# Kernel optimization log

Measured on AMD Instinct MI355X. Metric: run time of the kernel, lower is better.

## Reference

```python
import jax, jax.numpy as jnp
import numpy as np

N, E, D_IN, D, H, L, D_EMB, T = 4096, 131072, 72, 256, 8, 2, 128, 5
HD = D // H
LN_EPS = 1e-5


def _linear(x, w, b):
    # torch Linear: w is [out, in]
    return x @ w.T + b


def _layernorm(x, g, b):
    mu = jnp.mean(x, axis=-1, keepdims=True)
    var = jnp.var(x, axis=-1, keepdims=True)
    return (x - mu) * jax.lax.rsqrt(var + LN_EPS) * g + b


def _gps_layer(x, edge_index, p):
    src, dst = edge_index[0], edge_index[1]
    # GINConv: sum-aggregate neighbor messages, then MLP((1+eps)*x + agg)
    agg = jax.ops.segment_sum(x[src], dst, num_segments=N)
    h = (1.0 + p['gin_eps']) * x + agg
    h = _linear(jax.nn.elu(_linear(h, p['mlp_w1'], p['mlp_b1'])), p['mlp_w2'], p['mlp_b2'])
    h = jax.nn.elu(_layernorm(h, p['ln1_g'], p['ln1_b']))
    x = x + h

    # global multi-head self-attention over all N nodes (seq len = N)
    qkv = x @ p['attn_in_w'].T + p['attn_in_b']  # [N, 3D]
    q, k, v = jnp.split(qkv, 3, axis=-1)
    q = q.reshape(N, H, HD)
    k = k.reshape(N, H, HD)
    v = v.reshape(N, H, HD)
    scores = jnp.einsum('nhd,mhd->hnm', q, k) / np.sqrt(HD).astype(np.float32)
    attn = jax.nn.softmax(scores, axis=-1)
    o = jnp.einsum('hnm,mhd->nhd', attn, v).reshape(N, D)
    o = _linear(o, p['attn_out_w'], p['attn_out_b'])
    o = _layernorm(o, p['ln2_g'], p['ln2_b'])
    x = x + o

    # FFN (dim -> 2*dim -> dim, GELU)
    f = _linear(jax.nn.gelu(_linear(x, p['ffn_w1'], p['ffn_b1'])), p['ffn_w2'], p['ffn_b2'])
    f = _layernorm(f, p['ln3_g'], p['ln3_b'])
    return x + f


def setup_inputs() -> dict:
    key = jax.random.key(0)
    ks = iter(jax.random.split(key, 64))

    def w(shape, fan_in):
        return jax.random.normal(next(ks), shape, jnp.float32) * (1.0 / np.sqrt(fan_in))

    inp = {
        'x': jax.random.normal(next(ks), (N, D_IN), jnp.float32),
        'edge_index': jax.random.randint(next(ks), (2, E), 0, N, jnp.int64),
        'in_w': w((D, D_IN), D_IN), 'in_b': jnp.zeros((D,), jnp.float32),
        'head_w1': w((D_EMB, D), D), 'head_b1': jnp.zeros((D_EMB,), jnp.float32),
        'head_w2': w((T, D_EMB), D_EMB), 'head_b2': jnp.zeros((T,), jnp.float32),
    }
    # stacked per-layer params, leading axis L
    inp['mlp_w1'] = w((L, D, D), D); inp['mlp_b1'] = jnp.zeros((L, D), jnp.float32)
    inp['mlp_w2'] = w((L, D, D), D); inp['mlp_b2'] = jnp.zeros((L, D), jnp.float32)
    inp['gin_eps'] = jnp.zeros((L,), jnp.float32)
    inp['ln1_g'] = jnp.ones((L, D), jnp.float32); inp['ln1_b'] = jnp.zeros((L, D), jnp.float32)
    inp['attn_in_w'] = w((L, 3 * D, D), D); inp['attn_in_b'] = jnp.zeros((L, 3 * D), jnp.float32)
    inp['attn_out_w'] = w((L, D, D), D); inp['attn_out_b'] = jnp.zeros((L, D), jnp.float32)
    inp['ln2_g'] = jnp.ones((L, D), jnp.float32); inp['ln2_b'] = jnp.zeros((L, D), jnp.float32)
    inp['ffn_w1'] = w((L, 2 * D, D), D); inp['ffn_b1'] = jnp.zeros((L, 2 * D), jnp.float32)
    inp['ffn_w2'] = w((L, D, 2 * D), 2 * D); inp['ffn_b2'] = jnp.zeros((L, D), jnp.float32)
    inp['ln3_g'] = jnp.ones((L, D), jnp.float32); inp['ln3_b'] = jnp.zeros((L, D), jnp.float32)
    return inp


PER_LAYER = ['mlp_w1', 'mlp_b1', 'mlp_w2', 'mlp_b2', 'gin_eps', 'ln1_g', 'ln1_b',
             'attn_in_w', 'attn_in_b', 'attn_out_w', 'attn_out_b', 'ln2_g', 'ln2_b',
             'ffn_w1', 'ffn_b1', 'ffn_w2', 'ffn_b2', 'ln3_g', 'ln3_b']


def reference(x, edge_index, in_w, in_b, head_w1, head_b1, head_w2, head_b2,
              mlp_w1, mlp_b1, mlp_w2, mlp_b2, gin_eps, ln1_g, ln1_b,
              attn_in_w, attn_in_b, attn_out_w, attn_out_b, ln2_g, ln2_b,
              ffn_w1, ffn_b1, ffn_w2, ffn_b2, ln3_g, ln3_b):
    stacked = dict(mlp_w1=mlp_w1, mlp_b1=mlp_b1, mlp_w2=mlp_w2, mlp_b2=mlp_b2,
                   gin_eps=gin_eps, ln1_g=ln1_g, ln1_b=ln1_b,
                   attn_in_w=attn_in_w, attn_in_b=attn_in_b,
                   attn_out_w=attn_out_w, attn_out_b=attn_out_b,
                   ln2_g=ln2_g, ln2_b=ln2_b, ffn_w1=ffn_w1, ffn_b1=ffn_b1,
                   ffn_w2=ffn_w2, ffn_b2=ffn_b2, ln3_g=ln3_g, ln3_b=ln3_b)
    h = jax.nn.elu(_linear(x, in_w, in_b))  # input_proj (dropout/noise off in eval)
    for l in range(L):
        p = {k: v[l] for k, v in stacked.items()}
        h = _gps_layer(h, edge_index, p)
    out = _linear(jax.nn.elu(_linear(h, head_w1, head_b1)), head_w2, head_b2)
    return out
```

## Files before the change

kernel.cpp:

```cpp
#include <hip/hip_runtime.h>
#include <hip/hip_bf16.h>
#include <math.h>

#define NN 4096
#define NE 131072
#define DIM 256
#define NHEAD 8
#define HD 32

typedef __attribute__((ext_vector_type(8))) short short8v;
typedef __attribute__((ext_vector_type(4))) float f32x4;
#define MFMA16(a, b, c) __builtin_amdgcn_mfma_f32_16x16x32_bf16(a, b, c, 0, 0, 0)

__device__ __forceinline__ float elu_f(float v){ return v > 0.f ? v : expm1f(v); }
__device__ __forceinline__ float gelu_f(float v){
  const float c = 0.7978845608028654f;
  float t = tanhf(c * (v + 0.044715f * v * v * v));
  return 0.5f * v * (1.f + t);
}
__device__ __forceinline__ unsigned short f2bf(float f) {
  unsigned int u = __builtin_bit_cast(unsigned int, f);
  u += 0x7FFFu + ((u >> 16) & 1u);
  return (unsigned short)(u >> 16);
}
__device__ __forceinline__ float bf2f(unsigned short u) {
  return __builtin_bit_cast(float, (unsigned int)u << 16);
}
__device__ __forceinline__ unsigned int pk2c(float a, float b) {
  __hip_bfloat162 h = __float22bfloat162_rn(float2{a, b});
  unsigned int r;
  __builtin_memcpy(&r, &h, 4);
  return r;
}

__global__ void zero_counts(int* __restrict__ counts) {
  int i = blockIdx.x * 256 + threadIdx.x;
  if (i < NN) counts[i] = 0;
}

__global__ void count_edges(const int* __restrict__ ei, int* __restrict__ counts) {
  int e = blockIdx.x * 256 + threadIdx.x;
  if (e < NE) atomicAdd(&counts[ei[NE + e]], 1);
}

__global__ __launch_bounds__(1024) void scan_offsets(const int* __restrict__ counts,
                                                     int* __restrict__ offs,
                                                     int* __restrict__ cursor) {
  __shared__ int tmp[1024];
  int t = threadIdx.x;
  int base = t * 4;
  int c0 = counts[base], c1 = counts[base+1], c2 = counts[base+2], c3 = counts[base+3];
  int tsum = c0 + c1 + c2 + c3;
  tmp[t] = tsum;
  __syncthreads();
  for (int d = 1; d < 1024; d <<= 1) {
    int v = (t >= d) ? tmp[t - d] : 0;
    __syncthreads();
    tmp[t] += v;
    __syncthreads();
  }
  int excl = tmp[t] - tsum;
  offs[base]   = excl;           cursor[base]   = excl;
  offs[base+1] = excl + c0;      cursor[base+1] = excl + c0;
  offs[base+2] = excl + c0 + c1; cursor[base+2] = excl + c0 + c1;
  offs[base+3] = excl + c0 + c1 + c2; cursor[base+3] = excl + c0 + c1 + c2;
  if (t == 1023) offs[NN] = tmp[1023];
}

__global__ void scatter_edges(const int* __restrict__ ei, int* __restrict__ cursor,
                              int* __restrict__ esrc) {
  int e = blockIdx.x * 256 + threadIdx.x;
  if (e < NE) {
    int d = ei[NE + e];
    int pos = atomicAdd(&cursor[d], 1);
    esrc[pos] = ei[e];
  }
}

__global__ __launch_bounds__(256) void gin_agg(const int* __restrict__ offs,
                                               const int* __restrict__ esrc,
                                               const unsigned short* __restrict__ xb,
                                               const float* __restrict__ eps_p, int l,
                                               unsigned short* __restrict__ aggb) {
  int n = blockIdx.x, c = threadIdx.x;
  int e0 = offs[n], e1 = offs[n + 1];
  float acc = 0.f;
  for (int e = e0; e < e1; e++) acc += bf2f(xb[(size_t)esrc[e] * DIM + c]);
  float eps = eps_p[l];
  aggb[(size_t)n * DIM + c] = f2bf((1.f + eps) * bf2f(xb[(size_t)n * DIM + c]) + acc);
}

template<int ACT, int WF32, int WBF16, int QSCALE, int BK>
__global__ __launch_bounds__(256) void gemm_mfma(
    const unsigned short* __restrict__ A, const unsigned short* __restrict__ W,
    const float* __restrict__ bias, float* __restrict__ Cf,
    unsigned short* __restrict__ Cb, int M, int N, int K)
{
  __shared__ __align__(16) unsigned short As[2][64][BK + 8];
  __shared__ __align__(16) unsigned short Ws[2][32][BK + 8];
  constexpr int CPR = BK / 8;
  constexpr int ACH = 64 * CPR;
  constexpr int WCH = 32 * CPR;
  constexpr int NA = (ACH + 255) / 256;
  constexpr int NW = (WCH + 255) / 256;
  int t = threadIdx.x;
  int w = t >> 6, lane = t & 63, lo = lane & 15, g = lane >> 4;
  int wm = w & 1, wn = w >> 1;
  int bn = blockIdx.x * 32, bm = blockIdx.y * 64;

  f32x4 acc0 = {0.f, 0.f, 0.f, 0.f};
  f32x4 acc1 = {0.f, 0.f, 0.f, 0.f};
  short8v pa[NA], pw[NW];

  auto LOADG = [&](int k0) {
    #pragma unroll
    for (int i = 0; i < NA; i++) {
      int cc = i * 256 + t;
      int row = cc / CPR, off = (cc % CPR) * 8;
      pa[i] = *(const short8v*)(A + (size_t)(bm + row) * K + k0 + off);
    }
    #pragma unroll
    for (int i = 0; i < NW; i++) {
      int cc = i * 256 + t;
      if (cc < WCH) {
        int row = cc / CPR, off = (cc % CPR) * 8;
        pw[i] = *(const short8v*)(W + (size_t)(bn + row) * K + k0 + off);
      }
    }
  };
  auto STORE = [&](int b) {
    #pragma unroll
    for (int i = 0; i < NA; i++) {
      int cc = i * 256 + t;
      int row = cc / CPR, off = (cc % CPR) * 8;
      *(short8v*)&As[b][row][off] = pa[i];
    }
    #pragma unroll
    for (int i = 0; i < NW; i++) {
      int cc = i * 256 + t;
      if (cc < WCH) {
        int row = cc / CPR, off = (cc % CPR) * 8;
        *(short8v*)&Ws[b][row][off] = pw[i];
      }
    }
  };

  LOADG(0);
  STORE(0);
  __syncthreads();

  int buf = 0;
  for (int k0 = 0; k0 < K; k0 += BK) {
    bool more = (k0 + BK < K);
    if (more) LOADG(k0 + BK);
    #pragma unroll
    for (int ks = 0; ks < BK; ks += 32) {
      short8v a0 = *(const short8v*)&As[buf][wm * 32 + lo][ks + 8 * g];
      short8v a1 = *(const short8v*)&As[buf][wm * 32 + 16 + lo][ks + 8 * g];
      short8v b0 = *(const short8v*)&Ws[buf][wn * 16 + lo][ks + 8 * g];
      acc0 = MFMA16(a0, b0, acc0);
      acc1 = MFMA16(a1, b0, acc1);
    }
    if (more) STORE(buf ^ 1);
    __syncthreads();
    buf ^= 1;
  }

  #pragma unroll
  for (int mi = 0; mi < 2; mi++) {
    f32x4 av = (mi == 0) ? acc0 : acc1;
    #pragma unroll
    for (int r = 0; r < 4; r++) {
      int row = bm + wm * 32 + mi * 16 + 4 * g + r;
      int col = bn + wn * 16 + lo;
      float v = av[r] + bias[col];
      if (ACT == 1) v = elu_f(v);
      if (ACT == 2) v = gelu_f(v);
      if (QSCALE) { if (col < 256) v *= 0.17677669529663687f; }
      if (WF32) Cf[(size_t)row * N + col] = v;
      if (WBF16) Cb[(size_t)row * N + col] = f2bf(v);
    }
  }
}

template<int ACT>
__global__ __launch_bounds__(256) void ln_act_add(const float* __restrict__ in,
                                                  const float* __restrict__ g,
                                                  const float* __restrict__ b,
                                                  float* __restrict__ x,
                                                  unsigned short* __restrict__ xb) {
  int rowb = blockIdx.x;
  int c = threadIdx.x;
  float v = in[(size_t)rowb * DIM + c];
  float s = v, s2 = v * v;
  #pragma unroll
  for (int off = 32; off >= 1; off >>= 1) {
    s  += __shfl_xor(s,  off, 64);
    s2 += __shfl_xor(s2, off, 64);
  }
  __shared__ float ws1[4], ws2[4];
  int w = threadIdx.x >> 6, lane = threadIdx.x & 63;
  if (lane == 0) { ws1[w] = s; ws2[w] = s2; }
  __syncthreads();
  s  = ws1[0] + ws1[1] + ws1[2] + ws1[3];
  s2 = ws2[0] + ws2[1] + ws2[2] + ws2[3];
  float mean = s * (1.f / DIM);
  float var = s2 * (1.f / DIM) - mean * mean;
  float r = rsqrtf(var + 1e-5f);
  float o = (v - mean) * r * g[c] + b[c];
  if (ACT == 1) o = elu_f(o);
  float nx = x[(size_t)rowb * DIM + c] + o;
  x[(size_t)rowb * DIM + c] = nx;
  xb[(size_t)rowb * DIM + c] = f2bf(nx);
}

__global__ __launch_bounds__(256) void vt_transpose(const unsigned short* __restrict__ tbb,
                                                    unsigned short* __restrict__ VT) {
  __shared__ unsigned short lds[128][33];
  int h = blockIdx.y;
  int nb = blockIdx.x * 128;
  int tid = threadIdx.x;
  int r8 = tid >> 5, d = tid & 31;
  #pragma unroll
  for (int i = 0; i < 16; i++) {
    int n = i * 8 + r8;
    lds[n][d] = tbb[(size_t)(nb + n) * 768 + 512 + h * 32 + d];
  }
  __syncthreads();
  int dd = tid >> 7, j = tid & 127;
  #pragma unroll
  for (int i = 0; i < 16; i++) {
    int d2 = i * 2 + dd;
    VT[((size_t)h * 32 + d2) * 4096 + nb + j] = lds[j][d2];
  }
}

__global__ __launch_bounds__(256) void attn_mfma_split(
    const unsigned short* __restrict__ qkvb, const unsigned short* __restrict__ VT,
    float* __restrict__ po, float* __restrict__ ml, int kspan) {
  __shared__ __align__(16) unsigned short Ks[2][64][40];
  __shared__ __align__(16) unsigned short Vs[2][32][72];
  int tid = threadIdx.x;
  int w = tid >> 6, lane = tid & 63;
  int lo = lane & 15, g = lane >> 4;
  int h = blockIdx.y;
  int s = blockIdx.z;
  int qb = blockIdx.x * 64 + w * 16;
  int k_lo = s * kspan, k_hi = k_lo + kspan;

  int krow = tid >> 2, kq = (tid & 3) * 8;
  int vrow = tid >> 3, vo = (tid & 7) * 8;
  const unsigned short* Kg = qkvb + 256 + h * 32;
  const unsigned short* Vg = VT + ((size_t)(h * 32 + vrow)) * 4096;

  short8v qf = *(const short8v*)(qkvb + (size_t)(qb + lo) * 768 + h * 32 + 8 * g);

  f32x4 acc0 = {0.f, 0.f, 0.f, 0.f};
  f32x4 acc1 = {0.f, 0.f, 0.f, 0.f};
  float m = -1e30f, l = 0.f;
  const f32x4 zf = {0.f, 0.f, 0.f, 0.f};

  {
    short8v rk0 = *(const short8v*)(Kg + (size_t)(k_lo + krow) * 768 + kq);
    short8v rv0 = *(const short8v*)(Vg + k_lo + vo);
    *(short8v*)&Ks[0][krow][kq] = rk0;
    *(short8v*)&Vs[0][vrow][vo] = rv0;
  }
  __syncthreads();

  int buf = 0;
  for (int kb = k_lo; kb < k_hi; kb += 64) {
    short8v rk, rv;
    bool more = (kb + 64 < k_hi);
    if (more) {
      rk = *(const short8v*)(Kg + (size_t)(kb + 64 + krow) * 768 + kq);
      rv = *(const short8v*)(Vg + kb + 64 + vo);
    }

    short8v kA0 = *(const short8v*)&Ks[buf][lo][8 * g];
    short8v kA1 = *(const short8v*)&Ks[buf][16 + lo][8 * g];
    short8v kA2 = *(const short8v*)&Ks[buf][32 + lo][8 * g];
    short8v kA3 = *(const short8v*)&Ks[buf][48 + lo][8 * g];
    f32x4 s0_ = MFMA16(kA0, qf, zf);
    f32x4 s1_ = MFMA16(kA1, qf, zf);
    f32x4 s2_ = MFMA16(kA2, qf, zf);
    f32x4 s3_ = MFMA16(kA3, qf, zf);

    float ta_ = fmaxf(fmaxf(fmaxf(s0_[0],s0_[1]), fmaxf(s0_[2],s0_[3])),
                      fmaxf(fmaxf(s1_[0],s1_[1]), fmaxf(s1_[2],s1_[3])));
    float tb_ = fmaxf(fmaxf(fmaxf(s2_[0],s2_[1]), fmaxf(s2_[2],s2_[3])),
                      fmaxf(fmaxf(s3_[0],s3_[1]), fmaxf(s3_[2],s3_[3])));
    float t_ = fmaxf(ta_, tb_);
    t_ = fmaxf(t_, __shfl_xor(t_, 16, 64));
    t_ = fmaxf(t_, __shfl_xor(t_, 32, 64));
    if (!__all(t_ <= m)) {
      float nm_ = fmaxf(m, t_);
      float f_ = __expf(m - nm_);
      m = nm_; l *= f_;
      acc0[0]*=f_; acc0[1]*=f_; acc0[2]*=f_; acc0[3]*=f_;
      acc1[0]*=f_; acc1[1]*=f_; acc1[2]*=f_; acc1[3]*=f_;
    }
    float p0_=__expf(s0_[0]-m), p1_=__expf(s0_[1]-m), p2_=__expf(s0_[2]-m), p3_=__expf(s0_[3]-m);
    float p4_=__expf(s1_[0]-m), p5_=__expf(s1_[1]-m), p6_=__expf(s1_[2]-m), p7_=__expf(s1_[3]-m);
    float p8_=__expf(s2_[0]-m), p9_=__expf(s2_[1]-m), pA_=__expf(s2_[2]-m), pB_=__expf(s2_[3]-m);
    float pC_=__expf(s3_[0]-m), pD_=__expf(s3_[1]-m), pE_=__expf(s3_[2]-m), pF_=__expf(s3_[3]-m);
    l += ((((p0_+p1_)+(p2_+p3_)) + ((p4_+p5_)+(p6_+p7_))) +
          (((p8_+p9_)+(pA_+pB_)) + ((pC_+pD_)+(pE_+pF_))));

    uint4 uA_ = { pk2c(p0_,p1_), pk2c(p2_,p3_), pk2c(p4_,p5_), pk2c(p6_,p7_) };
    uint4 uB_ = { pk2c(p8_,p9_), pk2c(pA_,pB_), pk2c(pC_,pD_), pk2c(pE_,pF_) };
    short8v pbA_ = __builtin_bit_cast(short8v, uA_);
    short8v pbB_ = __builtin_bit_cast(short8v, uB_);

    short4 Wa0 = *(const short4*)&Vs[buf][lo][4 * g];
    short4 Wa1 = *(const short4*)&Vs[buf][lo][16 + 4 * g];
    short4 Wa2 = *(const short4*)&Vs[buf][lo][32 + 4 * g];
    short4 Wa3 = *(const short4*)&Vs[buf][lo][48 + 4 * g];
    short4 Xa0 = *(const short4*)&Vs[buf][16 + lo][4 * g];
    short4 Xa1 = *(const short4*)&Vs[buf][16 + lo][16 + 4 * g];
    short4 Xa2 = *(const short4*)&Vs[buf][16 + lo][32 + 4 * g];
    short4 Xa3 = *(const short4*)&Vs[buf][16 + lo][48 + 4 * g];
    short8v va0_ = {Wa0.x,Wa0.y,Wa0.z,Wa0.w, Wa1.x,Wa1.y,Wa1.z,Wa1.w};
    short8v va1_ = {Wa2.x,Wa2.y,Wa2.z,Wa2.w, Wa3.x,Wa3.y,Wa3.z,Wa3.w};
    short8v vb0_ = {Xa0.x,Xa0.y,Xa0.z,Xa0.w, Xa1.x,Xa1.y,Xa1.z,Xa1.w};
    short8v vb1_ = {Xa2.x,Xa2.y,Xa2.z,Xa2.w, Xa3.x,Xa3.y,Xa3.z,Xa3.w};
    acc0 = MFMA16(va0_, pbA_, acc0);
    acc0 = MFMA16(va1_, pbB_, acc0);
    acc1 = MFMA16(vb0_, pbA_, acc1);
    acc1 = MFMA16(vb1_, pbB_, acc1);

    if (more) {
      *(short8v*)&Ks[buf ^ 1][krow][kq] = rk;
      *(short8v*)&Vs[buf ^ 1][vrow][vo] = rv;
    }
    __syncthreads();
    buf ^= 1;
  }

  l += __shfl_xor(l, 16, 64);
  l += __shfl_xor(l, 32, 64);

  int q = qb + lo;
  float* pr = po + ((size_t)s * NN + q) * DIM + h * 32 + 4 * g;
  *(f32x4*)pr = acc0;
  *(f32x4*)(pr + 16) = acc1;
  if (g == 0) {
    float2* mlp = (float2*)(ml + (((size_t)s * NN + q) * NHEAD + h) * 2);
    *mlp = float2{m, l};
  }
}

__global__ __launch_bounds__(256) void attn_merge(const float* __restrict__ po,
                                                  const float* __restrict__ ml,
                                                  unsigned short* __restrict__ attb, int S) {
  int q = blockIdx.x;
  int c = threadIdx.x;
  int h = c >> 5;
  float M = -1e30f;
  for (int s = 0; s < S; s++)
    M = fmaxf(M, ml[(((size_t)s * NN + q) * NHEAD + h) * 2]);
  float L = 0.f, O = 0.f;
  for (int s = 0; s < S; s++) {
    const float* mlp = ml + (((size_t)s * NN + q) * NHEAD + h) * 2;
    float e = __expf(mlp[0] - M);
    L += e * mlp[1];
    O += e * po[((size_t)s * NN + q) * DIM + c];
  }
  attb[(size_t)q * DIM + c] = f2bf(O / L);
}

#define WO0 0
#define WO1 131072
#define WO2 262144
#define WO3 655360
#define WO4 786432
#define WO5 1048576
#define WO6 1310720
#define WTOT 1343488
#define WBLK 1312
#define XPBLK 1536
#define WPBLK 96
__global__ __launch_bounds__(256) void prep_convert(
    const float* __restrict__ s0, const float* __restrict__ s1,
    const float* __restrict__ s2, const float* __restrict__ s3,
    const float* __restrict__ s4, const float* __restrict__ s5,
    const float* __restrict__ s6, unsigned short* __restrict__ dst,
    const float* __restrict__ x_in, unsigned short* __restrict__ xinb,
    const float* __restrict__ in_w, unsigned short* __restrict__ inwb) {
  int bid = blockIdx.x;
  if (bid < WBLK) {
    int i4 = (bid * 256 + threadIdx.x) * 4;
    if (i4 >= WTOT) return;
    const float* src; int loc;
    if      (i4 < WO1) { src = s0; loc = i4 - WO0; }
    else if (i4 < WO2) { src = s1; loc = i4 - WO1; }
    else if (i4 < WO3) { src = s2; loc = i4 - WO2; }
    else if (i4 < WO4) { src = s3; loc = i4 - WO3; }
    else if (i4 < WO5) { src = s4; loc = i4 - WO4; }
    else if (i4 < WO6) { src = s5; loc = i4 - WO5; }
    else               { src = s6; loc = i4 - WO6; }
    float4 v = *(const float4*)(src + loc);
    ushort4 o;
    o.x = f2bf(v.x); o.y = f2bf(v.y); o.z = f2bf(v.z); o.w = f2bf(v.w);
    *(ushort4*)(dst + i4) = o;
  } else if (bid < WBLK + XPBLK) {
    int idx = (bid - WBLK) * 256 + threadIdx.x;
    int row = idx / 96, col = idx - row * 96;
    xinb[idx] = (col < 72) ? f2bf(x_in[row * 72 + col]) : (unsigned short)0;
  } else {
    int idx = (bid - WBLK - XPBLK) * 256 + threadIdx.x;
    int row = idx / 96, col = idx - row * 96;
    inwb[idx] = (col < 72) ? f2bf(in_w[row * 72 + col]) : (unsigned short)0;
  }
}

__global__ void head2_kernel(const float* __restrict__ e, const float* __restrict__ w,
                             const float* __restrict__ b, float* __restrict__ out) {
  int idx = blockIdx.x * 256 + threadIdx.x;
  if (idx >= NN * 5) return;
  int rowi = idx / 5, col = idx % 5;
  float s = b[col];
  const float* ep = e + (size_t)rowi * 128;
  const float* wp = w + (size_t)col * 128;
  #pragma unroll 16
  for (int k = 0; k < 128; k++) s += ep[k] * wp[k];
  out[idx] = s;
}

extern "C" void kernel_launch(void* const* d_in, const int* in_sizes, int n_in,
                              void* d_out, int out_size, void* d_ws, size_t ws_size,
                              hipStream_t stream) {
  const float* x_in   = (const float*)d_in[0];
  const int*   ei     = (const int*)  d_in[1];
  const float* in_w   = (const float*)d_in[2];
  const float* in_b   = (const float*)d_in[3];
  const float* head_w1= (const float*)d_in[4];
  const float* head_b1= (const float*)d_in[5];
  const float* head_w2= (const float*)d_in[6];
  const float* head_b2= (const float*)d_in[7];
  const float* mlp_w1 = (const float*)d_in[8];
  const float* mlp_b1 = (const float*)d_in[9];
  const float* mlp_w2 = (const float*)d_in[10];
  const float* mlp_b2 = (const float*)d_in[11];
  const float* gin_eps= (const float*)d_in[12];
  const float* ln1_g  = (const float*)d_in[13];
  const float* ln1_b  = (const float*)d_in[14];
  const float* attn_in_w = (const float*)d_in[15];
  const float* attn_in_b = (const float*)d_in[16];
  const float* attn_out_w= (const float*)d_in[17];
  const float* attn_out_b= (const float*)d_in[18];
  const float* ln2_g  = (const float*)d_in[19];
  const float* ln2_b  = (const float*)d_in[20];
  const float* ffn_w1 = (const float*)d_in[21];
  const float* ffn_b1 = (const float*)d_in[22];
  const float* ffn_w2 = (const float*)d_in[23];
  const float* ffn_b2 = (const float*)d_in[24];
  const float* ln3_g  = (const float*)d_in[25];
  const float* ln3_b  = (const float*)d_in[26];

  float* ws = (float*)d_ws;
  float* x    = ws;
  float* t2   = x  + (size_t)NN * DIM;
  float* he   = t2 + (size_t)NN * DIM;
  unsigned short* xb   = (unsigned short*)(he + (size_t)NN * 128);
  unsigned short* tbb  = xb   + (size_t)NN * DIM;
  unsigned short* aggb = tbb  + (size_t)NN * 768;
  unsigned short* attb = aggb + (size_t)NN * DIM;
  unsigned short* VT   = attb + (size_t)NN * DIM;
  unsigned short* xinb = VT   + (size_t)NN * DIM;
  unsigned short* inwb = xinb + (size_t)NN * 96;
  unsigned short* warena = inwb + 256 * 96;
  int* counts = (int*)(warena + WTOT);
  int* offs   = counts + NN;
  int* cursor = offs + NN + 1;
  int* esrc   = cursor + NN;
  float* po   = (float*)(esrc + NE);
  size_t used_f = (size_t)(po - ws);
  int S = 1;
  for (int cand = 8; cand >= 2; cand >>= 1) {
    size_t need = (used_f + (size_t)cand * NN * DIM + (size_t)cand * NN * NHEAD * 2) * 4;
    if (ws_size >= need) { S = cand; break; }
  }
  float* ml = po + (size_t)S * NN * DIM;
  int kspan = NN / S;

  const unsigned short* w_mlp1 = warena + WO0;
  const unsigned short* w_mlp2 = warena + WO1;
  const unsigned short* w_qkv  = warena + WO2;
  const unsigned short* w_aout = warena + WO3;
  const unsigned short* w_ffn1 = warena + WO4;
  const unsigned short* w_ffn2 = warena + WO5;
  const unsigned short* w_h1   = warena + WO6;

  zero_counts<<<16, 256, 0, stream>>>(counts);
  count_edges<<<NE / 256, 256, 0, stream>>>(ei, counts);
  scan_offsets<<<1, 1024, 0, stream>>>(counts, offs, cursor);
  scatter_edges<<<NE / 256, 256, 0, stream>>>(ei, cursor, esrc);

  prep_convert<<<WBLK + XPBLK + WPBLK, 256, 0, stream>>>(
      mlp_w1, mlp_w2, attn_in_w, attn_out_w, ffn_w1, ffn_w2, head_w1, warena,
      x_in, xinb, in_w, inwb);

  gemm_mfma<1,1,1,0,32><<<dim3(DIM/32, NN/64), 256, 0, stream>>>(xinb, inwb, in_b, x, xb,
                                                                 NN, DIM, 96);

  for (int l = 0; l < 2; l++) {
    gin_agg<<<NN, 256, 0, stream>>>(offs, esrc, xb, gin_eps, l, aggb);
    gemm_mfma<1,0,1,0,64><<<dim3(8, 64), 256, 0, stream>>>(aggb, w_mlp1 + (size_t)l*65536,
                                                           mlp_b1 + l*DIM, nullptr, tbb,
                                                           NN, DIM, DIM);
    gemm_mfma<0,1,0,0,64><<<dim3(8, 64), 256, 0, stream>>>(tbb, w_mlp2 + (size_t)l*65536,
                                                           mlp_b2 + l*DIM, t2, nullptr,
                                                           NN, DIM, DIM);
    ln_act_add<1><<<NN, 256, 0, stream>>>(t2, ln1_g + l*DIM, ln1_b + l*DIM, x, xb);

    gemm_mfma<0,0,1,1,64><<<dim3(24, 64), 256, 0, stream>>>(xb, w_qkv + (size_t)l*196608,
                                                            attn_in_b + l*768, nullptr, tbb,
                                                            NN, 768, DIM);
    vt_transpose<<<dim3(32, 8), 256, 0, stream>>>(tbb, VT);
    attn_mfma_split<<<dim3(64, NHEAD, S), 256, 0, stream>>>(tbb, VT, po, ml, kspan);
    attn_merge<<<NN, 256, 0, stream>>>(po, ml, attb, S);
    gemm_mfma<0,1,0,0,64><<<dim3(8, 64), 256, 0, stream>>>(attb, w_aout + (size_t)l*65536,
                                                           attn_out_b + l*DIM, t2, nullptr,
                                                           NN, DIM, DIM);
    ln_act_add<0><<<NN, 256, 0, stream>>>(t2, ln2_g + l*DIM, ln2_b + l*DIM, x, xb);

    gemm_mfma<2,0,1,0,64><<<dim3(16, 64), 256, 0, stream>>>(xb, w_ffn1 + (size_t)l*131072,
                                                            ffn_b1 + l*512, nullptr, tbb,
                                                            NN, 512, DIM);
    gemm_mfma<0,1,0,0,64><<<dim3(8, 64), 256, 0, stream>>>(tbb, w_ffn2 + (size_t)l*131072,
                                                           ffn_b2 + l*DIM, t2, nullptr,
                                                           NN, DIM, 512);
    ln_act_add<0><<<NN, 256, 0, stream>>>(t2, ln3_g + l*DIM, ln3_b + l*DIM, x, xb);
  }

  gemm_mfma<1,1,0,0,64><<<dim3(4, 64), 256, 0, stream>>>(xb, w_h1, head_b1, he, nullptr,
                                                         NN, 128, DIM);
  head2_kernel<<<(NN * 5 + 255) / 256, 256, 0, stream>>>(he, head_w2, head_b2, (float*)d_out);
}
```

Before: 347.2 us.

## Fuse V transpose into QKV GEMM epilogue and widen attention blocks to 512 threads

The QKV projection GEMM now writes the V columns straight into the transposed VT layout as 4-element vector stores, which removes the separate vt_transpose kernel and its extra read/write pass. The attention kernel moves to 512-thread blocks covering 128 queries each, with half the threads loading K tiles and the other half loading V tiles, so each staged K/V tile is shared by twice as many queries. The maximum key-split factor S drops from 8 to 4, which cuts partial-output traffic and merge work but leaves fewer blocks for parallelism.

```diff
diff --git a/kernel.cpp b/kernel.cpp
--- a/kernel.cpp
+++ b/kernel.cpp
@@ -90,11 +90,12 @@
   aggb[(size_t)n * DIM + c] = f2bf((1.f + eps) * bf2f(xb[(size_t)n * DIM + c]) + acc);
 }
 
-template<int ACT, int WF32, int WBF16, int QSCALE, int BK>
+template<int ACT, int WF32, int WBF16, int QSCALE, int BK, int WVT = 0>
 __global__ __launch_bounds__(256) void gemm_mfma(
     const unsigned short* __restrict__ A, const unsigned short* __restrict__ W,
     const float* __restrict__ bias, float* __restrict__ Cf,
-    unsigned short* __restrict__ Cb, int M, int N, int K)
+    unsigned short* __restrict__ Cb, int M, int N, int K,
+    unsigned short* __restrict__ VTout = nullptr)
 {
   __shared__ __align__(16) unsigned short As[2][64][BK + 8];
   __shared__ __align__(16) unsigned short Ws[2][32][BK + 8];
@@ -169,16 +170,25 @@
   #pragma unroll
   for (int mi = 0; mi < 2; mi++) {
     f32x4 av = (mi == 0) ? acc0 : acc1;
-    #pragma unroll
-    for (int r = 0; r < 4; r++) {
-      int row = bm + wm * 32 + mi * 16 + 4 * g + r;
-      int col = bn + wn * 16 + lo;
-      float v = av[r] + bias[col];
-      if (ACT == 1) v = elu_f(v);
-      if (ACT == 2) v = gelu_f(v);
-      if (QSCALE) { if (col < 256) v *= 0.17677669529663687f; }
-      if (WF32) Cf[(size_t)row * N + col] = v;
-      if (WBF16) Cb[(size_t)row * N + col] = f2bf(v);
+    int col = bn + wn * 16 + lo;
+    int rbase = bm + wm * 32 + mi * 16 + 4 * g;
+    if (WVT && col >= 512) {
+      ushort4 o;
+      float v0 = av[0] + bias[col], v1 = av[1] + bias[col];
+      float v2 = av[2] + bias[col], v3 = av[3] + bias[col];
+      o.x = f2bf(v0); o.y = f2bf(v1); o.z = f2bf(v2); o.w = f2bf(v3);
+      *(ushort4*)(VTout + (size_t)(col - 512) * 4096 + rbase) = o;
+    } else {
+      #pragma unroll
+      for (int r = 0; r < 4; r++) {
+        int row = rbase + r;
+        float v = av[r] + bias[col];
+        if (ACT == 1) v = elu_f(v);
+        if (ACT == 2) v = gelu_f(v);
+        if (QSCALE) { if (col < 256) v *= 0.17677669529663687f; }
+        if (WF32) Cf[(size_t)row * N + col] = v;
+        if (WBF16) Cb[(size_t)row * N + col] = f2bf(v);
+      }
     }
   }
 }
@@ -214,28 +224,7 @@
   xb[(size_t)rowb * DIM + c] = f2bf(nx);
 }
 
-__global__ __launch_bounds__(256) void vt_transpose(const unsigned short* __restrict__ tbb,
-                                                    unsigned short* __restrict__ VT) {
-  __shared__ unsigned short lds[128][33];
-  int h = blockIdx.y;
-  int nb = blockIdx.x * 128;
-  int tid = threadIdx.x;
-  int r8 = tid >> 5, d = tid & 31;
-  #pragma unroll
-  for (int i = 0; i < 16; i++) {
-    int n = i * 8 + r8;
-    lds[n][d] = tbb[(size_t)(nb + n) * 768 + 512 + h * 32 + d];
-  }
-  __syncthreads();
-  int dd = tid >> 7, j = tid & 127;
-  #pragma unroll
-  for (int i = 0; i < 16; i++) {
-    int d2 = i * 2 + dd;
-    VT[((size_t)h * 32 + d2) * 4096 + nb + j] = lds[j][d2];
-  }
-}
-
-__global__ __launch_bounds__(256) void attn_mfma_split(
+__global__ __launch_bounds__(512) void attn_mfma_split(
     const unsigned short* __restrict__ qkvb, const unsigned short* __restrict__ VT,
     float* __restrict__ po, float* __restrict__ ml, int kspan) {
   __shared__ __align__(16) unsigned short Ks[2][64][40];
@@ -245,11 +234,13 @@
   int lo = lane & 15, g = lane >> 4;
   int h = blockIdx.y;
   int s = blockIdx.z;
-  int qb = blockIdx.x * 64 + w * 16;
+  int qb = blockIdx.x * 128 + w * 16;
   int k_lo = s * kspan, k_hi = k_lo + kspan;
 
+  bool isK = tid < 256;
   int krow = tid >> 2, kq = (tid & 3) * 8;
-  int vrow = tid >> 3, vo = (tid & 7) * 8;
+  int vtid = tid & 255;
+  int vrow = vtid >> 3, vo = (vtid & 7) * 8;
   const unsigned short* Kg = qkvb + 256 + h * 32;
   const unsigned short* Vg = VT + ((size_t)(h * 32 + vrow)) * 4096;
 
@@ -261,20 +252,23 @@
   const f32x4 zf = {0.f, 0.f, 0.f, 0.f};
 
   {
-    short8v rk0 = *(const short8v*)(Kg + (size_t)(k_lo + krow) * 768 + kq);
-    short8v rv0 = *(const short8v*)(Vg + k_lo + vo);
-    *(short8v*)&Ks[0][krow][kq] = rk0;
-    *(short8v*)&Vs[0][vrow][vo] = rv0;
+    if (isK) {
+      short8v rk0 = *(const short8v*)(Kg + (size_t)(k_lo + krow) * 768 + kq);
+      *(short8v*)&Ks[0][krow][kq] = rk0;
+    } else {
+      short8v rv0 = *(const short8v*)(Vg + k_lo + vo);
+      *(short8v*)&Vs[0][vrow][vo] = rv0;
+    }
   }
   __syncthreads();
 
   int buf = 0;
   for (int kb = k_lo; kb < k_hi; kb += 64) {
-    short8v rk, rv;
+    short8v rg;
     bool more = (kb + 64 < k_hi);
     if (more) {
-      rk = *(const short8v*)(Kg + (size_t)(kb + 64 + krow) * 768 + kq);
-      rv = *(const short8v*)(Vg + kb + 64 + vo);
+      if (isK) rg = *(const short8v*)(Kg + (size_t)(kb + 64 + krow) * 768 + kq);
+      else     rg = *(const short8v*)(Vg + kb + 64 + vo);
     }
 
     short8v kA0 = *(const short8v*)&Ks[buf][lo][8 * g];
@@ -330,8 +324,8 @@
     acc1 = MFMA16(vb1_, pbB_, acc1);
 
     if (more) {
-      *(short8v*)&Ks[buf ^ 1][krow][kq] = rk;
-      *(short8v*)&Vs[buf ^ 1][vrow][vo] = rv;
+      if (isK) *(short8v*)&Ks[buf ^ 1][krow][kq] = rg;
+      else     *(short8v*)&Vs[buf ^ 1][vrow][vo] = rg;
     }
     __syncthreads();
     buf ^= 1;
@@ -477,7 +471,7 @@
   float* po   = (float*)(esrc + NE);
   size_t used_f = (size_t)(po - ws);
   int S = 1;
-  for (int cand = 8; cand >= 2; cand >>= 1) {
+  for (int cand = 4; cand >= 2; cand >>= 1) {
     size_t need = (used_f + (size_t)cand * NN * DIM + (size_t)cand * NN * NHEAD * 2) * 4;
     if (ws_size >= need) { S = cand; break; }
   }
@@ -514,11 +508,10 @@
                                                            NN, DIM, DIM);
     ln_act_add<1><<<NN, 256, 0, stream>>>(t2, ln1_g + l*DIM, ln1_b + l*DIM, x, xb);
 
-    gemm_mfma<0,0,1,1,64><<<dim3(24, 64), 256, 0, stream>>>(xb, w_qkv + (size_t)l*196608,
-                                                            attn_in_b + l*768, nullptr, tbb,
-                                                            NN, 768, DIM);
-    vt_transpose<<<dim3(32, 8), 256, 0, stream>>>(tbb, VT);
-    attn_mfma_split<<<dim3(64, NHEAD, S), 256, 0, stream>>>(tbb, VT, po, ml, kspan);
+    gemm_mfma<0,0,1,1,64,1><<<dim3(24, 64), 256, 0, stream>>>(xb, w_qkv + (size_t)l*196608,
+                                                              attn_in_b + l*768, nullptr, tbb,
+                                                              NN, 768, DIM, VT);
+    attn_mfma_split<<<dim3(32, NHEAD, S), 512, 0, stream>>>(tbb, VT, po, ml, kspan);
     attn_merge<<<NN, 256, 0, stream>>>(po, ml, attb, S);
     gemm_mfma<0,1,0,0,64><<<dim3(8, 64), 256, 0, stream>>>(attb, w_aout + (size_t)l*65536,
                                                            attn_out_b + l*DIM, t2, nullptr,
```

New measurement: 325.2 us. -6.4%, faster.
